# Kernel tuning notes

Measured on AMD Instinct MI355X. Metric: run time of the kernel, lower is better.

Reference implementation:

```python
import jax, jax.numpy as jnp
import numpy as np
import math

DIM = 1024
NUM_HEADS = 16
HEAD_DIM = DIM // NUM_HEADS  # 64
LAYER_IDX = 12
LAMBDA_INIT = 0.8 - 0.6 * math.exp(-0.3 * (LAYER_IDX - 1))
LN_EPS = 1e-5


def setup_inputs() -> dict:
    key = jax.random.key(0)
    ks = jax.random.split(key, 11)
    B, S = 2, 2048
    x = jax.random.normal(ks[0], (B, S, DIM), dtype=jnp.float32)
    s = 1.0 / math.sqrt(DIM)
    Wq = jax.random.normal(ks[1], (DIM, 2 * DIM), dtype=jnp.float32) * s
    Wk = jax.random.normal(ks[2], (DIM, 2 * DIM), dtype=jnp.float32) * s
    Wv = jax.random.normal(ks[3], (DIM, DIM), dtype=jnp.float32) * s
    Wo = jax.random.normal(ks[4], (DIM, DIM), dtype=jnp.float32) * s
    lambda_q1 = jax.random.normal(ks[5], (HEAD_DIM,), dtype=jnp.float32) * 0.1
    lambda_k1 = jax.random.normal(ks[6], (HEAD_DIM,), dtype=jnp.float32) * 0.1
    lambda_q2 = jax.random.normal(ks[7], (HEAD_DIM,), dtype=jnp.float32) * 0.1
    lambda_k2 = jax.random.normal(ks[8], (HEAD_DIM,), dtype=jnp.float32) * 0.1
    gamma = jnp.ones((DIM,), dtype=jnp.float32)
    beta = jnp.zeros((DIM,), dtype=jnp.float32)
    return {"x": x, "Wq": Wq, "Wk": Wk, "Wv": Wv, "Wo": Wo,
            "lambda_q1": lambda_q1, "lambda_k1": lambda_k1,
            "lambda_q2": lambda_q2, "lambda_k2": lambda_k2,
            "gamma": gamma, "beta": beta}


def reference(x, Wq, Wk, Wv, Wo, lambda_q1, lambda_k1, lambda_q2, lambda_k2, gamma, beta):
    B, S, _ = x.shape
    scaling = HEAD_DIM ** (-0.5)
    # projections: [B,S,H,2d] / [B,S,H,d] -> [B,H,S,*]
    Q = (x @ Wq).reshape(B, S, NUM_HEADS, 2 * HEAD_DIM).transpose(0, 2, 1, 3)
    K = (x @ Wk).reshape(B, S, NUM_HEADS, 2 * HEAD_DIM).transpose(0, 2, 1, 3)
    V = (x @ Wv).reshape(B, S, NUM_HEADS, HEAD_DIM).transpose(0, 2, 1, 3)
    # lambda scalar
    lamb = (jnp.exp(jnp.sum(lambda_q1 * lambda_k1))
            - jnp.exp(jnp.sum(lambda_q2 * lambda_k2)) + LAMBDA_INIT)
    Q1, Q2 = jnp.split(Q, 2, axis=-1)
    K1, K2 = jnp.split(K, 2, axis=-1)
    A1 = jnp.einsum('bhqd,bhkd->bhqk', Q1, K1) * scaling
    A2 = jnp.einsum('bhqd,bhkd->bhqk', Q2, K2) * scaling
    attn = jax.nn.softmax(A1, axis=-1) - lamb * jax.nn.softmax(A2, axis=-1)
    out = jnp.einsum('bhqk,bhkd->bhqd', attn, V)  # [B,H,S,d]
    out = out.transpose(0, 2, 1, 3).reshape(B, S, DIM)
    out = out @ Wo
    # LayerNorm
    mu = jnp.mean(out, axis=-1, keepdims=True)
    var = jnp.var(out, axis=-1, keepdims=True)
    out = (out - mu) * jax.lax.rsqrt(var + LN_EPS) * gamma + beta
    return out
```

## Files before the change

kernel.cpp:

```cpp
#include <hip/hip_runtime.h>
#include <hip/hip_bf16.h>

typedef short bf16x8 __attribute__((ext_vector_type(8)));
typedef float f32x4 __attribute__((ext_vector_type(4)));
typedef unsigned short us4v __attribute__((ext_vector_type(4)));
typedef unsigned int uint2v __attribute__((ext_vector_type(2)));

#define DEV static __device__ __forceinline__

DEV float bf2f(unsigned short u){ unsigned int x = ((unsigned int)u)<<16; float f; __builtin_memcpy(&f,&x,4); return f; }
DEV unsigned short f2bf(float f){ unsigned int x; __builtin_memcpy(&x,&f,4); x = (x + 0x7fffu + ((x>>16)&1u)) >> 16; return (unsigned short)x; }

DEV unsigned int pack_trunc(float lo, float hi){
  unsigned int a, b;
  __builtin_memcpy(&a, &lo, 4);
  __builtin_memcpy(&b, &hi, 4);
  return (b & 0xffff0000u) | (a >> 16);
}

DEV void stor(unsigned short* p, float v){ *p = f2bf(v); }
DEV void stor(float* p, float v){ *p = v; }

#if __has_builtin(__builtin_amdgcn_exp2f)
DEV float fexp2(float x){ return __builtin_amdgcn_exp2f(x); }
#else
DEV float fexp2(float x){ return exp2f(x); }
#endif

#if __has_builtin(__builtin_amdgcn_permlane32_swap)
DEV uint2v pl32(unsigned int a, unsigned int b){ return __builtin_amdgcn_permlane32_swap(a, b, false, false); }
#else
DEV uint2v pl32(unsigned int a, unsigned int b){
  unsigned int sa = (unsigned int)__shfl_xor((int)a, 32);
  unsigned int sb = (unsigned int)__shfl_xor((int)b, 32);
  bool hi = (threadIdx.x & 32) != 0;
  uint2v r; r[0] = hi ? sb : a; r[1] = hi ? b : sa; return r;
}
#endif
#if __has_builtin(__builtin_amdgcn_permlane16_swap)
DEV uint2v pl16(unsigned int a, unsigned int b){ return __builtin_amdgcn_permlane16_swap(a, b, false, false); }
#else
DEV uint2v pl16(unsigned int a, unsigned int b){
  unsigned int sa = (unsigned int)__shfl_xor((int)a, 16);
  unsigned int sb = (unsigned int)__shfl_xor((int)b, 16);
  bool hi = (threadIdx.x & 16) != 0;
  uint2v r; r[0] = hi ? sb : a; r[1] = hi ? b : sa; return r;
}
#endif

#define GLOAD_LDS16(gptr, lptr) \
  __builtin_amdgcn_global_load_lds((__attribute__((address_space(1))) void*)(gptr), \
      (__attribute__((address_space(3))) void*)(lptr), 16, 0, 0)

template<typename OutT>
__global__ __launch_bounds__(256) void gemm_bt(
    const unsigned short* __restrict__ A,
    const unsigned short* __restrict__ Bt,
    OutT* __restrict__ C, int M, int N, int K)
{
  __shared__ unsigned short As[128*32];
  __shared__ unsigned short Bs[128*32];
  const int tid = threadIdx.x;
  const int w = tid>>6, l = tid&63, g = l>>4, q = l&15;
  const int m0 = blockIdx.x*128, n0 = blockIdx.y*128;
  f32x4 acc[4][4];
  const f32x4 fz = {0.f,0.f,0.f,0.f};
  for (int i=0;i<4;i++) for(int j=0;j<4;j++) acc[i][j] = fz;
  for (int k0 = 0; k0 < K; k0 += 32) {
    __syncthreads();
    #pragma unroll
    for (int r = 0; r < 2; ++r) {
      int p = r*4096 + tid*16;
      int row = p>>6, colb = p&63;
      const char* ga = (const char*)(A  + (size_t)(m0+row)*K + k0) + colb;
      const char* gb = (const char*)(Bt + (size_t)(n0+row)*K + k0) + colb;
      GLOAD_LDS16(ga, (char*)As + r*4096 + w*1024);
      GLOAD_LDS16(gb, (char*)Bs + r*4096 + w*1024);
    }
    __syncthreads();
    bf16x8 af[4], bfr[4];
    #pragma unroll
    for (int i=0;i<4;i++){
      af[i]  = *(const bf16x8*)&As[((w>>1)*64 + i*16 + q)*32 + g*8];
      bfr[i] = *(const bf16x8*)&Bs[((w&1)*64 + i*16 + q)*32 + g*8];
    }
    #pragma unroll
    for (int i=0;i<4;i++)
      #pragma unroll
      for (int j=0;j<4;j++)
        acc[i][j] = __builtin_amdgcn_mfma_f32_16x16x32_bf16(af[i], bfr[j], acc[i][j], 0,0,0);
  }
  #pragma unroll
  for (int i=0;i<4;i++)
    #pragma unroll
    for (int j=0;j<4;j++)
      #pragma unroll
      for (int v=0;v<4;v++){
        int row = m0 + (w>>1)*64 + i*16 + g*4 + v;
        int col = n0 + (w&1)*64 + j*16 + q;
        stor(&C[(size_t)row*N + col], acc[i][j][v]);
      }
}

__global__ __launch_bounds__(256,2) void diff_attn(
    const unsigned short* __restrict__ Qp,
    const unsigned short* __restrict__ Kp,
    const unsigned short* __restrict__ Vt,
    const float* __restrict__ lambp,
    unsigned short* __restrict__ aout)
{
  const int LDQ = 5120;
  __shared__ unsigned short Ks[2][64*128];
  __shared__ unsigned short Vs[2][64*64];
  const int tid = threadIdx.x, w = tid>>6, l = tid&63, g = l>>4, q = l&15;
  const int qb = blockIdx.x, h = blockIdx.y, b = blockIdx.z;
  const int b2048 = b*2048;
  const int qrow0 = b2048 + qb*128 + w*32;
  const f32x4 fz = {0.f,0.f,0.f,0.f};
  const short one_bf = (short)0x3f80;
  const bf16x8 ones = {one_bf,one_bf,one_bf,one_bf,one_bf,one_bf,one_bf,one_bf};

  bf16x8 q1f[2][2], q2f[2][2];
  #pragma unroll
  for (int qh=0; qh<2; ++qh){
    const unsigned short* qp = Qp + (size_t)(qrow0 + qh*16 + q)*LDQ + h*128;
    #pragma unroll
    for (int kf=0;kf<2;kf++){
      q1f[qh][kf] = *(const bf16x8*)(qp + kf*32 + g*8);
      q2f[qh][kf] = *(const bf16x8*)(qp + 64 + kf*32 + g*8);
    }
  }
  f32x4 acc1[2][4], acc2[2][4];
  f32x4 acc_s1[2], acc_s2[2];
  #pragma unroll
  for (int qh=0;qh<2;qh++){
    acc_s1[qh]=fz; acc_s2[qh]=fz;
    #pragma unroll
    for (int i=0;i<4;i++){ acc1[qh][i]=fz; acc2[qh][i]=fz; }
  }

  auto STAGE = [&](int bb, int kt){
    #pragma unroll
    for (int ii=0; ii<4; ++ii){
      int krow = w*16 + ii*4 + (l>>4);
      int gr = (l&15) ^ (krow&7);
      const unsigned short* src = Kp + (size_t)(b2048 + kt + krow)*LDQ + h*128 + gr*8;
      GLOAD_LDS16(src, (char*)&Ks[bb][0] + (w*16 + ii*4)*256);
    }
    #pragma unroll
    for (int jj=0; jj<2; ++jj){
      int vrow = w*16 + jj*8 + (l>>3);
      int gr = (l&7) ^ (vrow&7);
      const unsigned short* src = Vt + (size_t)(h*64 + vrow)*4096 + b2048 + kt + gr*8;
      GLOAD_LDS16(src, (char*)&Vs[bb][0] + (w*16 + jj*8)*128);
    }
  };

  STAGE(0, 0);
  __syncthreads();

  for (int t=0; t<32; ++t) {
    const int bb = t & 1;
    if (t < 31) STAGE(bb^1, (t+1)*64);
    const int sw = q & 7;

    unsigned int c1[2][4][2], c2[2][4][2];
    #pragma unroll
    for (int fn=0; fn<4; ++fn) {
      const unsigned short* kr = &Ks[bb][(fn*16 + q)*128];
      bf16x8 kb0 = *(const bf16x8*)&kr[((0+g)^sw)*8];
      bf16x8 kb1 = *(const bf16x8*)&kr[((4+g)^sw)*8];
      bf16x8 kc0 = *(const bf16x8*)&kr[((8+g)^sw)*8];
      bf16x8 kc1 = *(const bf16x8*)&kr[((12+g)^sw)*8];
      f32x4 za[2], zc[2];
      __builtin_amdgcn_s_setprio(1);
      #pragma unroll
      for (int qh=0; qh<2; ++qh){
        f32x4 a = fz, c = fz;
        a = __builtin_amdgcn_mfma_f32_16x16x32_bf16(kb0, q1f[qh][0], a, 0,0,0);
        a = __builtin_amdgcn_mfma_f32_16x16x32_bf16(kb1, q1f[qh][1], a, 0,0,0);
        c = __builtin_amdgcn_mfma_f32_16x16x32_bf16(kc0, q2f[qh][0], c, 0,0,0);
        c = __builtin_amdgcn_mfma_f32_16x16x32_bf16(kc1, q2f[qh][1], c, 0,0,0);
        za[qh]=a; zc[qh]=c;
      }
      __builtin_amdgcn_s_setprio(0);
      #pragma unroll
      for (int qh=0; qh<2; ++qh){
        float e0 = fexp2(za[qh][0]), e1 = fexp2(za[qh][1]);
        float e2 = fexp2(za[qh][2]), e3 = fexp2(za[qh][3]);
        c1[qh][fn][0] = pack_trunc(e0,e1); c1[qh][fn][1] = pack_trunc(e2,e3);
        float f0 = fexp2(zc[qh][0]), f1 = fexp2(zc[qh][1]);
        float f2 = fexp2(zc[qh][2]), f3 = fexp2(zc[qh][3]);
        c2[qh][fn][0] = pack_trunc(f0,f1); c2[qh][fn][1] = pack_trunc(f2,f3);
      }
    }

    bf16x8 pa1[2][2], pa2[2][2];
    #pragma unroll
    for (int qh=0; qh<2; ++qh)
      #pragma unroll
      for (int kh=0; kh<2; ++kh){
        unsigned int* u1 = (unsigned int*)&pa1[qh][kh];
        unsigned int* u2 = (unsigned int*)&pa2[qh][kh];
        #pragma unroll
        for (int j=0;j<2;j++){
          uint2v d = pl32(c1[qh][2*kh][j], c1[qh][2*kh+1][j]);
          uint2v e = pl16(d[0], d[1]);
          u1[j] = e[0]; u1[2+j] = e[1];
          uint2v d2 = pl32(c2[qh][2*kh][j], c2[qh][2*kh+1][j]);
          uint2v e2 = pl16(d2[0], d2[1]);
          u2[j] = e2[0]; u2[2+j] = e2[1];
        }
      }

    __builtin_amdgcn_s_setprio(1);
    #pragma unroll
    for (int kh=0; kh<2; ++kh){
      #pragma unroll
      for (int qh=0; qh<2; ++qh){
        acc_s1[qh] = __builtin_amdgcn_mfma_f32_16x16x32_bf16(pa1[qh][kh], ones, acc_s1[qh], 0,0,0);
        acc_s2[qh] = __builtin_amdgcn_mfma_f32_16x16x32_bf16(pa2[qh][kh], ones, acc_s2[qh], 0,0,0);
      }
      #pragma unroll
      for (int fd=0; fd<4; ++fd){
        bf16x8 vb = *(const bf16x8*)&Vs[bb][(fd*16+q)*64 + ((kh*4+g)^sw)*8];
        #pragma unroll
        for (int qh=0; qh<2; ++qh){
          acc1[qh][fd] = __builtin_amdgcn_mfma_f32_16x16x32_bf16(pa1[qh][kh], vb, acc1[qh][fd], 0,0,0);
          acc2[qh][fd] = __builtin_amdgcn_mfma_f32_16x16x32_bf16(pa2[qh][kh], vb, acc2[qh][fd], 0,0,0);
        }
      }
    }
    __builtin_amdgcn_s_setprio(0);

    if (t < 31) __syncthreads();
  }

  float lamb = lambp[0];
  #pragma unroll
  for (int qh=0; qh<2; ++qh){
    float inv1[4], inv2[4];
    #pragma unroll
    for (int i=0;i<4;i++){
      inv1[i] = 1.0f/acc_s1[qh][i];
      inv2[i] = lamb/acc_s2[qh][i];
    }
    #pragma unroll
    for (int fd=0; fd<4; ++fd)
      #pragma unroll
      for (int i=0;i<4;i++){
        float val = acc1[qh][fd][i]*inv1[i] - acc2[qh][fd][i]*inv2[i];
        int row = qrow0 + qh*16 + g*4 + i;
        int col = h*64 + fd*16 + q;
        aout[(size_t)row*1024 + col] = f2bf(val);
      }
  }
}

__global__ __launch_bounds__(256) void f32_to_bf16_k(const float* __restrict__ in, unsigned short* __restrict__ out, int n){
  int i = (blockIdx.x*256 + threadIdx.x)*4;
  if (i >= n) return;
  float4 vv = *(const float4*)(in + i);
  us4v o; o[0]=f2bf(vv.x); o[1]=f2bf(vv.y); o[2]=f2bf(vv.z); o[3]=f2bf(vv.w);
  *(us4v*)(out + i) = o;
}

__global__ void transpose_f32_bf16(const float* __restrict__ in, unsigned short* __restrict__ out, int R, int C, float scale){
  __shared__ unsigned short t[32][33];
  int c0 = blockIdx.x*32, r0 = blockIdx.y*32;
  int x = threadIdx.x, y = threadIdx.y;
  #pragma unroll
  for (int d=0; d<32; d+=8) t[y+d][x] = f2bf(in[(size_t)(r0+y+d)*C + c0 + x] * scale);
  __syncthreads();
  #pragma unroll
  for (int d=0; d<32; d+=8) out[(size_t)(c0+y+d)*R + r0 + x] = t[x][y+d];
}

__global__ void transpose_bf16_ld(const unsigned short* __restrict__ in, unsigned short* __restrict__ out, int R, int C, int ldin){
  __shared__ unsigned short t[32][33];
  int c0 = blockIdx.x*32, r0 = blockIdx.y*32;
  int x = threadIdx.x, y = threadIdx.y;
  #pragma unroll
  for (int d=0; d<32; d+=8) t[y+d][x] = in[(size_t)(r0+y+d)*ldin + c0 + x];
  __syncthreads();
  #pragma unroll
  for (int d=0; d<32; d+=8) out[(size_t)(c0+y+d)*R + r0 + x] = t[x][y+d];
}

__global__ void lamb_k(const float* lq1, const float* lk1, const float* lq2, const float* lk2, float* out){
  int i = threadIdx.x;
  float a = lq1[i]*lk1[i], c = lq2[i]*lk2[i];
  #pragma unroll
  for (int o=32;o>0;o>>=1){ a += __shfl_down(a,o); c += __shfl_down(c,o); }
  if (i==0) out[0] = expf(a) - expf(c) + 0.7778700995592560f;
}

__global__ __launch_bounds__(256) void ln_k(const float* __restrict__ in, const float* __restrict__ gam,
                                            const float* __restrict__ bet, float* __restrict__ out){
  int row = blockIdx.x, t = threadIdx.x;
  const float4* rp = (const float4*)(in + (size_t)row*1024);
  float4 v4 = rp[t];
  float s = v4.x+v4.y+v4.z+v4.w;
  float ss = v4.x*v4.x+v4.y*v4.y+v4.z*v4.z+v4.w*v4.w;
  #pragma unroll
  for (int o=1;o<64;o<<=1){ s += __shfl_xor(s,o); ss += __shfl_xor(ss,o); }
  __shared__ float red[8];
  int w = t>>6, l = t&63;
  if (l==0){ red[w]=s; red[4+w]=ss; }
  __syncthreads();
  s = red[0]+red[1]+red[2]+red[3];
  ss = red[4]+red[5]+red[6]+red[7];
  float mean = s*(1.0f/1024.0f);
  float var = ss*(1.0f/1024.0f) - mean*mean;
  float rstd = rsqrtf(var + 1e-5f);
  float4 gv = ((const float4*)gam)[t], bv = ((const float4*)bet)[t];
  float4 o;
  o.x = (v4.x-mean)*rstd*gv.x + bv.x;
  o.y = (v4.y-mean)*rstd*gv.y + bv.y;
  o.z = (v4.z-mean)*rstd*gv.z + bv.z;
  o.w = (v4.w-mean)*rstd*gv.w + bv.w;
  ((float4*)(out + (size_t)row*1024))[t] = o;
}

extern "C" void kernel_launch(void* const* d_in, const int* in_sizes, int n_in,
                              void* d_out, int out_size, void* d_ws, size_t ws_size,
                              hipStream_t stream) {
  const float* x     = (const float*)d_in[0];
  const float* Wq    = (const float*)d_in[1];
  const float* Wk    = (const float*)d_in[2];
  const float* Wv    = (const float*)d_in[3];
  const float* Wo    = (const float*)d_in[4];
  const float* lq1   = (const float*)d_in[5];
  const float* lk1   = (const float*)d_in[6];
  const float* lq2   = (const float*)d_in[7];
  const float* lk2   = (const float*)d_in[8];
  const float* gamma = (const float*)d_in[9];
  const float* beta  = (const float*)d_in[10];
  float* out = (float*)d_out;

  char* ws = (char*)d_ws;
  unsigned short* xb    = (unsigned short*)(ws);
  unsigned short* WcatT = (unsigned short*)(ws + 8388608);
  unsigned short* WoT   = (unsigned short*)(ws + 18874368);
  unsigned short* QKV   = (unsigned short*)(ws + 20971520);
  unsigned short* Vtb   = (unsigned short*)(ws + 62914560);
  unsigned short* AOb   = (unsigned short*)(ws + 71303168);
  float*          proj  = (float*)(ws + 79691776);
  float*          lambp = (float*)(ws + 96468992);

  const float QSCALE = 0.125f * 1.4426950408889634f;
  dim3 tb(32,8);
  f32_to_bf16_k<<<4096, 256, 0, stream>>>(x, xb, 4194304);
  transpose_f32_bf16<<<dim3(64,32), tb, 0, stream>>>(Wq, WcatT,             1024, 2048, QSCALE);
  transpose_f32_bf16<<<dim3(64,32), tb, 0, stream>>>(Wk, WcatT + 2048*1024, 1024, 2048, 1.0f);
  transpose_f32_bf16<<<dim3(32,32), tb, 0, stream>>>(Wv, WcatT + 4096*1024, 1024, 1024, 1.0f);
  transpose_f32_bf16<<<dim3(32,32), tb, 0, stream>>>(Wo, WoT, 1024, 1024, 1.0f);
  lamb_k<<<1, 64, 0, stream>>>(lq1, lk1, lq2, lk2, lambp);

  gemm_bt<unsigned short><<<dim3(32,40), 256, 0, stream>>>(xb, WcatT, QKV, 4096, 5120, 1024);
  transpose_bf16_ld<<<dim3(32,128), tb, 0, stream>>>(QKV + 4096, Vtb, 4096, 1024, 5120);

  diff_attn<<<dim3(16,16,2), 256, 0, stream>>>(QKV, QKV + 2048, Vtb, lambp, AOb);

  gemm_bt<float><<<dim3(32,8), 256, 0, stream>>>(AOb, WoT, proj, 4096, 1024, 1024);
  ln_k<<<4096, 256, 0, stream>>>(proj, gamma, beta, out);
}
```

Before: 201.7 us.

## Split diff-attention into per-softmax blocks and double-buffer GEMM LDS tiles

The attention kernel now launches separate blocks for each of the two softmax maps. Each block computes one normalized attention output, with half the K tile in LDS and half the accumulators, so more blocks can be resident per CU. A new combine kernel subtracts lambda times the second output from the first before the output projection, at the cost of extra global traffic and an additional rounding to bf16. Separately, the GEMM now double-buffers its LDS tiles so the next k-slice loads while MFMAs run on the current one.

```diff
diff --git a/kernel.cpp b/kernel.cpp
--- a/kernel.cpp
+++ b/kernel.cpp
@@ -58,37 +58,44 @@
     const unsigned short* __restrict__ Bt,
     OutT* __restrict__ C, int M, int N, int K)
 {
-  __shared__ unsigned short As[128*32];
-  __shared__ unsigned short Bs[128*32];
+  __shared__ unsigned short As[2][128*32];
+  __shared__ unsigned short Bs[2][128*32];
   const int tid = threadIdx.x;
   const int w = tid>>6, l = tid&63, g = l>>4, q = l&15;
   const int m0 = blockIdx.x*128, n0 = blockIdx.y*128;
   f32x4 acc[4][4];
   const f32x4 fz = {0.f,0.f,0.f,0.f};
   for (int i=0;i<4;i++) for(int j=0;j<4;j++) acc[i][j] = fz;
-  for (int k0 = 0; k0 < K; k0 += 32) {
-    __syncthreads();
+
+  auto STAGE = [&](int bb, int k0){
     #pragma unroll
     for (int r = 0; r < 2; ++r) {
       int p = r*4096 + tid*16;
       int row = p>>6, colb = p&63;
       const char* ga = (const char*)(A  + (size_t)(m0+row)*K + k0) + colb;
       const char* gb = (const char*)(Bt + (size_t)(n0+row)*K + k0) + colb;
-      GLOAD_LDS16(ga, (char*)As + r*4096 + w*1024);
-      GLOAD_LDS16(gb, (char*)Bs + r*4096 + w*1024);
-    }
-    __syncthreads();
+      GLOAD_LDS16(ga, (char*)&As[bb][0] + r*4096 + w*1024);
+      GLOAD_LDS16(gb, (char*)&Bs[bb][0] + r*4096 + w*1024);
+    }
+  };
+
+  STAGE(0, 0);
+  __syncthreads();
+  int bb = 0;
+  for (int k0 = 0; k0 < K; k0 += 32, bb ^= 1) {
+    if (k0 + 32 < K) STAGE(bb^1, k0+32);
     bf16x8 af[4], bfr[4];
     #pragma unroll
     for (int i=0;i<4;i++){
-      af[i]  = *(const bf16x8*)&As[((w>>1)*64 + i*16 + q)*32 + g*8];
-      bfr[i] = *(const bf16x8*)&Bs[((w&1)*64 + i*16 + q)*32 + g*8];
+      af[i]  = *(const bf16x8*)&As[bb][((w>>1)*64 + i*16 + q)*32 + g*8];
+      bfr[i] = *(const bf16x8*)&Bs[bb][((w&1)*64 + i*16 + q)*32 + g*8];
     }
     #pragma unroll
     for (int i=0;i<4;i++)
       #pragma unroll
       for (int j=0;j<4;j++)
         acc[i][j] = __builtin_amdgcn_mfma_f32_16x16x32_bf16(af[i], bfr[j], acc[i][j], 0,0,0);
+    if (k0 + 32 < K) __syncthreads();
   }
   #pragma unroll
   for (int i=0;i<4;i++)
@@ -102,50 +109,50 @@
       }
 }
 
-__global__ __launch_bounds__(256,2) void diff_attn(
+__global__ __launch_bounds__(256,4) void diff_attn(
     const unsigned short* __restrict__ Qp,
     const unsigned short* __restrict__ Kp,
     const unsigned short* __restrict__ Vt,
-    const float* __restrict__ lambp,
-    unsigned short* __restrict__ aout)
+    unsigned short* __restrict__ ao1,
+    unsigned short* __restrict__ ao2)
 {
   const int LDQ = 5120;
-  __shared__ unsigned short Ks[2][64*128];
+  __shared__ unsigned short Ks[2][64*64];
   __shared__ unsigned short Vs[2][64*64];
   const int tid = threadIdx.x, w = tid>>6, l = tid&63, g = l>>4, q = l&15;
-  const int qb = blockIdx.x, h = blockIdx.y, b = blockIdx.z;
+  const int qb = blockIdx.x, h = blockIdx.y;
+  const int s = blockIdx.z >> 1, b = blockIdx.z & 1;
   const int b2048 = b*2048;
   const int qrow0 = b2048 + qb*128 + w*32;
   const f32x4 fz = {0.f,0.f,0.f,0.f};
   const short one_bf = (short)0x3f80;
   const bf16x8 ones = {one_bf,one_bf,one_bf,one_bf,one_bf,one_bf,one_bf,one_bf};
-
-  bf16x8 q1f[2][2], q2f[2][2];
+  unsigned short* aout = s ? ao2 : ao1;
+
+  bf16x8 qf[2][2];
   #pragma unroll
   for (int qh=0; qh<2; ++qh){
-    const unsigned short* qp = Qp + (size_t)(qrow0 + qh*16 + q)*LDQ + h*128;
-    #pragma unroll
-    for (int kf=0;kf<2;kf++){
-      q1f[qh][kf] = *(const bf16x8*)(qp + kf*32 + g*8);
-      q2f[qh][kf] = *(const bf16x8*)(qp + 64 + kf*32 + g*8);
-    }
-  }
-  f32x4 acc1[2][4], acc2[2][4];
-  f32x4 acc_s1[2], acc_s2[2];
+    const unsigned short* qp = Qp + (size_t)(qrow0 + qh*16 + q)*LDQ + h*128 + s*64;
+    #pragma unroll
+    for (int kf=0;kf<2;kf++)
+      qf[qh][kf] = *(const bf16x8*)(qp + kf*32 + g*8);
+  }
+  f32x4 acc[2][4];
+  f32x4 acc_s[2];
   #pragma unroll
   for (int qh=0;qh<2;qh++){
-    acc_s1[qh]=fz; acc_s2[qh]=fz;
-    #pragma unroll
-    for (int i=0;i<4;i++){ acc1[qh][i]=fz; acc2[qh][i]=fz; }
+    acc_s[qh]=fz;
+    #pragma unroll
+    for (int i=0;i<4;i++) acc[qh][i]=fz;
   }
 
   auto STAGE = [&](int bb, int kt){
     #pragma unroll
-    for (int ii=0; ii<4; ++ii){
-      int krow = w*16 + ii*4 + (l>>4);
-      int gr = (l&15) ^ (krow&7);
-      const unsigned short* src = Kp + (size_t)(b2048 + kt + krow)*LDQ + h*128 + gr*8;
-      GLOAD_LDS16(src, (char*)&Ks[bb][0] + (w*16 + ii*4)*256);
+    for (int ii=0; ii<2; ++ii){
+      int krow = w*16 + ii*8 + (l>>3);
+      int gr = (l&7) ^ (krow&7);
+      const unsigned short* src = Kp + (size_t)(b2048 + kt + krow)*LDQ + h*128 + s*64 + gr*8;
+      GLOAD_LDS16(src, (char*)&Ks[bb][0] + (w*16 + ii*8)*128);
     }
     #pragma unroll
     for (int jj=0; jj<2; ++jj){
@@ -164,52 +171,40 @@
     if (t < 31) STAGE(bb^1, (t+1)*64);
     const int sw = q & 7;
 
-    unsigned int c1[2][4][2], c2[2][4][2];
+    unsigned int cc[2][4][2];
     #pragma unroll
     for (int fn=0; fn<4; ++fn) {
-      const unsigned short* kr = &Ks[bb][(fn*16 + q)*128];
+      const unsigned short* kr = &Ks[bb][(fn*16 + q)*64];
       bf16x8 kb0 = *(const bf16x8*)&kr[((0+g)^sw)*8];
       bf16x8 kb1 = *(const bf16x8*)&kr[((4+g)^sw)*8];
-      bf16x8 kc0 = *(const bf16x8*)&kr[((8+g)^sw)*8];
-      bf16x8 kc1 = *(const bf16x8*)&kr[((12+g)^sw)*8];
-      f32x4 za[2], zc[2];
+      f32x4 z[2];
       __builtin_amdgcn_s_setprio(1);
       #pragma unroll
       for (int qh=0; qh<2; ++qh){
-        f32x4 a = fz, c = fz;
-        a = __builtin_amdgcn_mfma_f32_16x16x32_bf16(kb0, q1f[qh][0], a, 0,0,0);
-        a = __builtin_amdgcn_mfma_f32_16x16x32_bf16(kb1, q1f[qh][1], a, 0,0,0);
-        c = __builtin_amdgcn_mfma_f32_16x16x32_bf16(kc0, q2f[qh][0], c, 0,0,0);
-        c = __builtin_amdgcn_mfma_f32_16x16x32_bf16(kc1, q2f[qh][1], c, 0,0,0);
-        za[qh]=a; zc[qh]=c;
+        f32x4 a = fz;
+        a = __builtin_amdgcn_mfma_f32_16x16x32_bf16(kb0, qf[qh][0], a, 0,0,0);
+        a = __builtin_amdgcn_mfma_f32_16x16x32_bf16(kb1, qf[qh][1], a, 0,0,0);
+        z[qh] = a;
       }
       __builtin_amdgcn_s_setprio(0);
       #pragma unroll
       for (int qh=0; qh<2; ++qh){
-        float e0 = fexp2(za[qh][0]), e1 = fexp2(za[qh][1]);
-        float e2 = fexp2(za[qh][2]), e3 = fexp2(za[qh][3]);
-        c1[qh][fn][0] = pack_trunc(e0,e1); c1[qh][fn][1] = pack_trunc(e2,e3);
-        float f0 = fexp2(zc[qh][0]), f1 = fexp2(zc[qh][1]);
-        float f2 = fexp2(zc[qh][2]), f3 = fexp2(zc[qh][3]);
-        c2[qh][fn][0] = pack_trunc(f0,f1); c2[qh][fn][1] = pack_trunc(f2,f3);
-      }
-    }
-
-    bf16x8 pa1[2][2], pa2[2][2];
+        cc[qh][fn][0] = pack_trunc(fexp2(z[qh][0]), fexp2(z[qh][1]));
+        cc[qh][fn][1] = pack_trunc(fexp2(z[qh][2]), fexp2(z[qh][3]));
+      }
+    }
+
+    bf16x8 pa[2][2];
     #pragma unroll
     for (int qh=0; qh<2; ++qh)
       #pragma unroll
       for (int kh=0; kh<2; ++kh){
-        unsigned int* u1 = (unsigned int*)&pa1[qh][kh];
-        unsigned int* u2 = (unsigned int*)&pa2[qh][kh];
+        unsigned int* u = (unsigned int*)&pa[qh][kh];
         #pragma unroll
         for (int j=0;j<2;j++){
-          uint2v d = pl32(c1[qh][2*kh][j], c1[qh][2*kh+1][j]);
+          uint2v d = pl32(cc[qh][2*kh][j], cc[qh][2*kh+1][j]);
           uint2v e = pl16(d[0], d[1]);
-          u1[j] = e[0]; u1[2+j] = e[1];
-          uint2v d2 = pl32(c2[qh][2*kh][j], c2[qh][2*kh+1][j]);
-          uint2v e2 = pl16(d2[0], d2[1]);
-          u2[j] = e2[0]; u2[2+j] = e2[1];
+          u[j] = e[0]; u[2+j] = e[1];
         }
       }
 
@@ -217,18 +212,14 @@
     #pragma unroll
     for (int kh=0; kh<2; ++kh){
       #pragma unroll
-      for (int qh=0; qh<2; ++qh){
-        acc_s1[qh] = __builtin_amdgcn_mfma_f32_16x16x32_bf16(pa1[qh][kh], ones, acc_s1[qh], 0,0,0);
-        acc_s2[qh] = __builtin_amdgcn_mfma_f32_16x16x32_bf16(pa2[qh][kh], ones, acc_s2[qh], 0,0,0);
-      }
+      for (int qh=0; qh<2; ++qh)
+        acc_s[qh] = __builtin_amdgcn_mfma_f32_16x16x32_bf16(pa[qh][kh], ones, acc_s[qh], 0,0,0);
       #pragma unroll
       for (int fd=0; fd<4; ++fd){
         bf16x8 vb = *(const bf16x8*)&Vs[bb][(fd*16+q)*64 + ((kh*4+g)^sw)*8];
         #pragma unroll
-        for (int qh=0; qh<2; ++qh){
-          acc1[qh][fd] = __builtin_amdgcn_mfma_f32_16x16x32_bf16(pa1[qh][kh], vb, acc1[qh][fd], 0,0,0);
-          acc2[qh][fd] = __builtin_amdgcn_mfma_f32_16x16x32_bf16(pa2[qh][kh], vb, acc2[qh][fd], 0,0,0);
-        }
+        for (int qh=0; qh<2; ++qh)
+          acc[qh][fd] = __builtin_amdgcn_mfma_f32_16x16x32_bf16(pa[qh][kh], vb, acc[qh][fd], 0,0,0);
       }
     }
     __builtin_amdgcn_s_setprio(0);
@@ -236,25 +227,35 @@
     if (t < 31) __syncthreads();
   }
 
-  float lamb = lambp[0];
   #pragma unroll
   for (int qh=0; qh<2; ++qh){
-    float inv1[4], inv2[4];
-    #pragma unroll
-    for (int i=0;i<4;i++){
-      inv1[i] = 1.0f/acc_s1[qh][i];
-      inv2[i] = lamb/acc_s2[qh][i];
-    }
+    float inv[4];
+    #pragma unroll
+    for (int i=0;i<4;i++) inv[i] = 1.0f/acc_s[qh][i];
     #pragma unroll
     for (int fd=0; fd<4; ++fd)
       #pragma unroll
       for (int i=0;i<4;i++){
-        float val = acc1[qh][fd][i]*inv1[i] - acc2[qh][fd][i]*inv2[i];
         int row = qrow0 + qh*16 + g*4 + i;
         int col = h*64 + fd*16 + q;
-        aout[(size_t)row*1024 + col] = f2bf(val);
-      }
-  }
+        aout[(size_t)row*1024 + col] = f2bf(acc[qh][fd][i]*inv[i]);
+      }
+  }
+}
+
+__global__ __launch_bounds__(256) void combine_k(
+    const unsigned short* __restrict__ a1, const unsigned short* __restrict__ a2,
+    const float* __restrict__ lambp, unsigned short* __restrict__ out, int n)
+{
+  int i = (blockIdx.x*256 + threadIdx.x)*8;
+  if (i >= n) return;
+  float lamb = lambp[0];
+  bf16x8 v1 = *(const bf16x8*)(a1+i), v2 = *(const bf16x8*)(a2+i);
+  bf16x8 o;
+  #pragma unroll
+  for (int e=0;e<8;e++)
+    o[e] = (short)f2bf(bf2f((unsigned short)v1[e]) - lamb*bf2f((unsigned short)v2[e]));
+  *(bf16x8*)(out+i) = o;
 }
 
 __global__ __launch_bounds__(256) void f32_to_bf16_k(const float* __restrict__ in, unsigned short* __restrict__ out, int n){
@@ -344,8 +345,10 @@
   unsigned short* WoT   = (unsigned short*)(ws + 18874368);
   unsigned short* QKV   = (unsigned short*)(ws + 20971520);
   unsigned short* Vtb   = (unsigned short*)(ws + 62914560);
-  unsigned short* AOb   = (unsigned short*)(ws + 71303168);
-  float*          proj  = (float*)(ws + 79691776);
+  unsigned short* AO1   = (unsigned short*)(ws + 71303168);
+  unsigned short* AO2   = (unsigned short*)(ws + 79691776);
+  unsigned short* AOc   = (unsigned short*)(ws + 88080384);
+  float*          proj  = (float*)(ws + 20971520);
   float*          lambp = (float*)(ws + 96468992);
 
   const float QSCALE = 0.125f * 1.4426950408889634f;
@@ -360,8 +363,9 @@
   gemm_bt<unsigned short><<<dim3(32,40), 256, 0, stream>>>(xb, WcatT, QKV, 4096, 5120, 1024);
   transpose_bf16_ld<<<dim3(32,128), tb, 0, stream>>>(QKV + 4096, Vtb, 4096, 1024, 5120);
 
-  diff_attn<<<dim3(16,16,2), 256, 0, stream>>>(QKV, QKV + 2048, Vtb, lambp, AOb);
-
-  gemm_bt<float><<<dim3(32,8), 256, 0, stream>>>(AOb, WoT, proj, 4096, 1024, 1024);
+  diff_attn<<<dim3(16,16,4), 256, 0, stream>>>(QKV, QKV + 2048, Vtb, AO1, AO2);
+  combine_k<<<2048, 256, 0, stream>>>(AO1, AO2, lambp, AOc, 4194304);
+
+  gemm_bt<float><<<dim3(32,8), 256, 0, stream>>>(AOc, WoT, proj, 4096, 1024, 1024);
   ln_k<<<4096, 256, 0, stream>>>(proj, gamma, beta, out);
 }
```

After: 243.0 us. 1.2x slower.
